# Kernel optimization log

Hardware: AMD Instinct MI355X
Metric: run time of the kernel (lower is better)

The kernel has to match this reference:

```python
import jax, jax.numpy as jnp
import numpy as np

B = 512     # graphs
NPG = 128   # nodes per graph
EPG = 2048  # edges per graph (avg degree 16)
IN = 128
HID = 128
K = 64      # ceil(0.5 * 128), SAGPooling ratio=0.5


def setup_inputs() -> dict:
    key = jax.random.key(0)
    ks = jax.random.split(key, 8)
    n_total = B * NPG
    x = jax.random.normal(ks[0], (n_total, IN), dtype=jnp.float32)
    # intra-graph random edges (PyG batching: edges never cross graphs)
    g = jnp.repeat(jnp.arange(B, dtype=jnp.int32), EPG)
    src = g * NPG + jax.random.randint(ks[1], (B * EPG,), 0, NPG, dtype=jnp.int32)
    dst = g * NPG + jax.random.randint(ks[2], (B * EPG,), 0, NPG, dtype=jnp.int32)
    edge_index = jnp.stack([src, dst], axis=0)
    batch = jnp.repeat(jnp.arange(B, dtype=jnp.int32), NPG)
    # params (glorot-ish scaling)
    W1 = jax.random.normal(ks[3], (IN, HID), dtype=jnp.float32) / np.sqrt(IN)
    b1 = jnp.zeros((HID,), dtype=jnp.float32)
    Ws = jax.random.normal(ks[4], (HID, 1), dtype=jnp.float32) / np.sqrt(HID)
    bs = jnp.zeros((1,), dtype=jnp.float32)
    Wlin = jax.random.normal(ks[5], (HID, HID), dtype=jnp.float32) / np.sqrt(HID)
    blin = jnp.zeros((HID,), dtype=jnp.float32)
    return {"x": x, "edge_index": edge_index, "batch": batch,
            "W1": W1, "b1": b1, "Ws": Ws, "bs": bs, "Wlin": Wlin, "blin": blin}


def _gcn_conv(x, src, dst, W, b, n):
    # PyG GCNConv: add self loops, symmetric deg^-1/2 norm, aggregate src->dst
    h = x @ W  # [n, out]
    loop = jnp.arange(n, dtype=src.dtype)
    s = jnp.concatenate([src, loop])
    d = jnp.concatenate([dst, loop])
    deg = jax.ops.segment_sum(jnp.ones(d.shape[0], dtype=x.dtype), d, num_segments=n)
    norm = jax.lax.rsqrt(deg)[s] * jax.lax.rsqrt(deg)[d]  # deg >= 1 via self loops
    msg = h[s] * norm[:, None]
    return jax.ops.segment_sum(msg, d, num_segments=n) + b


def reference(x, edge_index, batch, W1, b1, Ws, bs, Wlin, blin):
    n = x.shape[0]
    src, dst = edge_index[0], edge_index[1]
    # conv1 + relu
    h = jax.nn.relu(_gcn_conv(x, src, dst, W1, b1, n))  # [n, HID]
    # SAGPooling: score via GCNConv(HID -> 1)
    score = _gcn_conv(h, src, dst, Ws, bs, n)[:, 0]  # [n]
    # per-graph top-k on raw score (graphs are uniform NPG nodes -> dense top_k)
    score2 = score.reshape(B, NPG)
    top_v, top_i = jax.lax.top_k(score2, K)  # [B, K]
    h3 = h.reshape(B, NPG, HID)
    h_kept = jnp.take_along_axis(h3, top_i[:, :, None], axis=1)  # [B, K, HID]
    h_kept = h_kept * jnp.tanh(top_v)[:, :, None]  # x[perm] * tanh(score[perm])
    # global_mean_pool over kept nodes of each graph
    pooled = h_kept.mean(axis=1)  # [B, HID]
    return pooled @ Wlin + blin
```

## Files before the change

kernel.cpp:

```cpp
#include <hip/hip_runtime.h>
#include <math.h>

#define NPG  128
#define HID  128
#define KSEL 64
#define NT   256
#define HS   132
#define AS   17

typedef __attribute__((ext_vector_type(8))) __bf16 bfrag;
typedef __attribute__((ext_vector_type(4))) float f4;

static __device__ __forceinline__ __bf16 us2bf(unsigned short u) {
    union { unsigned short s; __bf16 b; } x; x.s = u; return x.b;
}
static __device__ __forceinline__ unsigned short bf2us(__bf16 b) {
    union { unsigned short s; __bf16 b; } x; x.b = b; return x.s;
}

__global__ __launch_bounds__(64) void wsplit_kernel(const float* __restrict__ W1,
                                                    bfrag* __restrict__ whi,
                                                    bfrag* __restrict__ wlo)
{
    const int b = blockIdx.x;
    const int ks = b >> 3, ct = b & 7;
    const int lane = threadIdx.x;
    const int n = lane & 15, quad = lane >> 4;
    bfrag h, l;
#pragma unroll
    for (int j = 0; j < 8; ++j) {
        const int k = ks * 32 + quad * 8 + j;
        float w = W1[k * HID + ct * 16 + n];
        __bf16 hh = (__bf16)w;
        h[j] = hh;
        l[j] = (__bf16)(w - (float)hh);
    }
    whi[b * 64 + lane] = h;
    wlo[b * 64 + lane] = l;
}

__global__ __launch_bounds__(NT, 2) void sagpool_fused(
    const float* __restrict__ x,
    const int*   __restrict__ esrc,
    const int*   __restrict__ edst,
    const bfrag* __restrict__ whi,
    const bfrag* __restrict__ wlo,
    const float* __restrict__ b1,
    const float* __restrict__ Ws,
    const float* __restrict__ bsp,
    const float* __restrict__ Wlin,
    const float* __restrict__ blin,
    float* __restrict__ out,
    int epg)
{
    __shared__ __align__(16) unsigned HpT[HID * HS];
    __shared__ __align__(16) unsigned AdjN[NPG * AS];
    __shared__ __align__(16) float rsl[NPG];
    __shared__ __align__(16) float spl[NPG];
    __shared__ __align__(16) float scl[NPG];
    __shared__ __align__(16) float wgt[NPG];
    __shared__ __align__(16) float pp[4 * HID];

    const int g = blockIdx.x, t = threadIdx.x;
    const int node0 = g * NPG;
    const long e0 = (long)g * epg;
    const int lane = t & 63, wv = t >> 6;
    const int n16 = lane & 15, quad = lane >> 4;

    int es[8], ed[8];
#pragma unroll
    for (int i = 0; i < 8; ++i) {
        int e = i * NT + t;
        es[i] = esrc[e0 + e] - node0;
        ed[i] = edst[e0 + e] - node0;
    }
    float4 xv[16];
    {
        const float* xw = x + (long)(node0 + wv * 32) * HID;
#pragma unroll
        for (int rt = 0; rt < 2; ++rt)
#pragma unroll
            for (int ks = 0; ks < 4; ++ks) {
                const float* xr = xw + (rt * 16 + n16) * HID + ks * 32 + quad * 8;
                xv[(rt * 4 + ks) * 2]     = *reinterpret_cast<const float4*>(xr);
                xv[(rt * 4 + ks) * 2 + 1] = *reinterpret_cast<const float4*>(xr + 4);
            }
    }
    float b1v[8], wsv[8];
#pragma unroll
    for (int ct = 0; ct < 8; ++ct) {
        b1v[ct] = b1[ct * 16 + n16];
        wsv[ct] = Ws[ct * 16 + n16];
    }
    const float bsv = bsp[0];

    for (int i = t; i < NPG * AS; i += NT) AdjN[i] = 0u;
    __syncthreads();
#pragma unroll
    for (int i = 0; i < 8; ++i)
        atomicAdd(&AdjN[ed[i] * AS + (es[i] >> 3)], 1u << ((es[i] & 7) * 4));
    __syncthreads();

    if (t < NPG) {
        unsigned* row = &AdjN[t * AS];
        row[t >> 3] += 1u << ((t & 7) * 4);
        unsigned sum = 0;
#pragma unroll
        for (int w = 0; w < 16; ++w) {
            unsigned u = row[w];
            unsigned b = (u & 0x0F0F0F0Fu) + ((u >> 4) & 0x0F0F0F0Fu);
            sum += (b * 0x01010101u) >> 24;
        }
        rsl[t] = rsqrtf((float)sum);
    }
    __syncthreads();

    bfrag ah[8], al[8];
#pragma unroll
    for (int r = 0; r < 8; ++r) {
        float4 a = xv[2 * r], b = xv[2 * r + 1];
        float vv[8] = {a.x, a.y, a.z, a.w, b.x, b.y, b.z, b.w};
#pragma unroll
        for (int j = 0; j < 8; ++j) {
            __bf16 hb = (__bf16)vv[j];
            ah[r][j] = hb;
            al[r][j] = (__bf16)(vv[j] - (float)hb);
        }
    }
    f4 acc[2][8];
#pragma unroll
    for (int rt = 0; rt < 2; ++rt)
#pragma unroll
        for (int ct = 0; ct < 8; ++ct) {
            acc[rt][ct].x = 0.f; acc[rt][ct].y = 0.f;
            acc[rt][ct].z = 0.f; acc[rt][ct].w = 0.f;
        }
#pragma unroll
    for (int ks = 0; ks < 4; ++ks)
#pragma unroll
        for (int ct = 0; ct < 8; ++ct) {
            bfrag bh = whi[(ks * 8 + ct) * 64 + lane];
            bfrag bl = wlo[(ks * 8 + ct) * 64 + lane];
#pragma unroll
            for (int rt = 0; rt < 2; ++rt) {
                const int r = rt * 4 + ks;
                acc[rt][ct] = __builtin_amdgcn_mfma_f32_16x16x32_bf16(ah[r], bh, acc[rt][ct], 0, 0, 0);
                acc[rt][ct] = __builtin_amdgcn_mfma_f32_16x16x32_bf16(al[r], bh, acc[rt][ct], 0, 0, 0);
                acc[rt][ct] = __builtin_amdgcn_mfma_f32_16x16x32_bf16(ah[r], bl, acc[rt][ct], 0, 0, 0);
                acc[rt][ct] = __builtin_amdgcn_mfma_f32_16x16x32_bf16(al[r], bl, acc[rt][ct], 0, 0, 0);
            }
        }

#pragma unroll
    for (int rt = 0; rt < 2; ++rt) {
        const int mb = wv * 32 + rt * 16 + quad * 4;
        f4 rs4 = *reinterpret_cast<const f4*>(&rsl[mb]);
#pragma unroll
        for (int ct = 0; ct < 8; ++ct) {
            uint4 st;
            unsigned pw[4];
#pragma unroll
            for (int reg = 0; reg < 4; ++reg) {
                float v = acc[rt][ct][reg] * rs4[reg];
                __bf16 hb = (__bf16)v;
                __bf16 lb = (__bf16)(v - (float)hb);
                pw[reg] = ((unsigned)bf2us(hb) << 16) | (unsigned)bf2us(lb);
            }
            st.x = pw[0]; st.y = pw[1]; st.z = pw[2]; st.w = pw[3];
            *reinterpret_cast<uint4*>(&HpT[(ct * 16 + n16) * HS + mb]) = st;
        }
    }
    __syncthreads();

    f4 hacc[2][8];
#pragma unroll
    for (int mt = 0; mt < 2; ++mt)
#pragma unroll
        for (int ct = 0; ct < 8; ++ct) {
            hacc[mt][ct].x = 0.f; hacc[mt][ct].y = 0.f;
            hacc[mt][ct].z = 0.f; hacc[mt][ct].w = 0.f;
        }
#pragma unroll
    for (int ks = 0; ks < 4; ++ks) {
        bfrag af[2];
#pragma unroll
        for (int mt = 0; mt < 2; ++mt) {
            unsigned w = AdjN[(wv * 32 + mt * 16 + n16) * AS + ks * 4 + quad];
#pragma unroll
            for (int j = 0; j < 8; ++j)
                af[mt][j] = (__bf16)(float)((w >> (4 * j)) & 15u);
        }
#pragma unroll
        for (int ct = 0; ct < 8; ++ct) {
            const unsigned* bp = &HpT[(ct * 16 + n16) * HS + ks * 32 + quad * 8];
            uint4 w0 = *reinterpret_cast<const uint4*>(bp);
            uint4 w1 = *reinterpret_cast<const uint4*>(bp + 4);
            unsigned ww[8] = {w0.x, w0.y, w0.z, w0.w, w1.x, w1.y, w1.z, w1.w};
            bfrag bh, bl;
#pragma unroll
            for (int j = 0; j < 8; ++j) {
                bh[j] = us2bf((unsigned short)(ww[j] >> 16));
                bl[j] = us2bf((unsigned short)(ww[j] & 0xFFFFu));
            }
#pragma unroll
            for (int mt = 0; mt < 2; ++mt) {
                hacc[mt][ct] = __builtin_amdgcn_mfma_f32_16x16x32_bf16(af[mt], bh, hacc[mt][ct], 0, 0, 0);
                hacc[mt][ct] = __builtin_amdgcn_mfma_f32_16x16x32_bf16(af[mt], bl, hacc[mt][ct], 0, 0, 0);
            }
        }
    }

    f4 rsm[2];
#pragma unroll
    for (int mt = 0; mt < 2; ++mt)
        rsm[mt] = *reinterpret_cast<const f4*>(&rsl[wv * 32 + mt * 16 + quad * 4]);
#pragma unroll
    for (int mt = 0; mt < 2; ++mt)
#pragma unroll
        for (int ct = 0; ct < 8; ++ct)
#pragma unroll
            for (int reg = 0; reg < 4; ++reg)
                hacc[mt][ct][reg] = fmaxf(hacc[mt][ct][reg] * rsm[mt][reg] + b1v[ct], 0.f);

    {
        float dot[2][4];
#pragma unroll
        for (int mt = 0; mt < 2; ++mt)
#pragma unroll
            for (int reg = 0; reg < 4; ++reg) dot[mt][reg] = 0.f;
#pragma unroll
        for (int ct = 0; ct < 8; ++ct)
#pragma unroll
            for (int mt = 0; mt < 2; ++mt)
#pragma unroll
                for (int reg = 0; reg < 4; ++reg)
                    dot[mt][reg] += hacc[mt][ct][reg] * wsv[ct];
#pragma unroll
        for (int d = 1; d < 16; d <<= 1)
#pragma unroll
            for (int mt = 0; mt < 2; ++mt)
#pragma unroll
                for (int reg = 0; reg < 4; ++reg)
                    dot[mt][reg] += __shfl_xor(dot[mt][reg], d, 64);
        if (n16 == 0) {
#pragma unroll
            for (int mt = 0; mt < 2; ++mt)
#pragma unroll
                for (int reg = 0; reg < 4; ++reg)
                    spl[wv * 32 + mt * 16 + quad * 4 + reg] = rsm[mt][reg] * dot[mt][reg];
        }
    }
    __syncthreads();

    if (t < NPG) {
        const unsigned* row = &AdjN[t * AS];
        float sc = 0.f;
#pragma unroll
        for (int w = 0; w < 16; ++w) {
            unsigned u = row[w];
            const float* sp = &spl[w * 8];
            sc += (float)(u & 15u)         * sp[0] + (float)((u >> 4)  & 15u) * sp[1]
                + (float)((u >> 8)  & 15u) * sp[2] + (float)((u >> 12) & 15u) * sp[3]
                + (float)((u >> 16) & 15u) * sp[4] + (float)((u >> 20) & 15u) * sp[5]
                + (float)((u >> 24) & 15u) * sp[6] + (float)(u >> 28)         * sp[7];
        }
        scl[t] = rsl[t] * sc + bsv;
    }
    __syncthreads();

    if (t < NPG) {
        float v = scl[t];
        int rank = 0;
        for (int j = 0; j < NPG; ++j) {
            float u = scl[j];
            rank += (u > v || (u == v && j < t)) ? 1 : 0;
        }
        wgt[t] = (rank < KSEL) ? tanhf(v) * (1.0f / KSEL) : 0.f;
    }
    __syncthreads();

    {
        float p[8];
        f4 wm[2];
#pragma unroll
        for (int mt = 0; mt < 2; ++mt)
            wm[mt] = *reinterpret_cast<const f4*>(&wgt[wv * 32 + mt * 16 + quad * 4]);
#pragma unroll
        for (int ct = 0; ct < 8; ++ct) {
            float s = 0.f;
#pragma unroll
            for (int mt = 0; mt < 2; ++mt)
#pragma unroll
                for (int reg = 0; reg < 4; ++reg)
                    s += wm[mt][reg] * hacc[mt][ct][reg];
            p[ct] = s;
        }
#pragma unroll
        for (int d = 16; d < 64; d <<= 1)
#pragma unroll
            for (int ct = 0; ct < 8; ++ct)
                p[ct] += __shfl_xor(p[ct], d, 64);
        if (quad == 0) {
#pragma unroll
            for (int ct = 0; ct < 8; ++ct)
                pp[wv * HID + ct * 16 + n16] = p[ct];
        }
    }
    __syncthreads();
    if (t < NPG)
        scl[t] = pp[t] + pp[HID + t] + pp[2 * HID + t] + pp[3 * HID + t];
    __syncthreads();

    {
        const int c = t & 127, hf = t >> 7;
        float s = 0.f;
        for (int k = hf * 64; k < hf * 64 + 64; ++k)
            s += scl[k] * Wlin[k * HID + c];
        pp[t] = s;
    }
    __syncthreads();
    if (t < NPG)
        out[(long)g * HID + t] = pp[t] + pp[t + 128] + blin[t];
}

extern "C" void kernel_launch(void* const* d_in, const int* in_sizes, int n_in,
                              void* d_out, int out_size, void* d_ws, size_t ws_size,
                              hipStream_t stream) {
    const float* x    = (const float*)d_in[0];
    const int*   ei   = (const int*)  d_in[1];
    const float* W1   = (const float*)d_in[3];
    const float* b1   = (const float*)d_in[4];
    const float* Ws   = (const float*)d_in[5];
    const float* bs   = (const float*)d_in[6];
    const float* Wlin = (const float*)d_in[7];
    const float* blin = (const float*)d_in[8];
    float* out = (float*)d_out;

    const int E = in_sizes[1] / 2;
    const int nnodes = in_sizes[0] / HID;
    const int B = nnodes / NPG;
    const int epg = E / B;

    bfrag* whi = reinterpret_cast<bfrag*>(d_ws);
    bfrag* wlo = whi + 32 * 64;

    wsplit_kernel<<<32, 64, 0, stream>>>(W1, whi, wlo);
    sagpool_fused<<<B, NT, 0, stream>>>(x, ei, ei + E, whi, wlo, b1, Ws, bs,
                                        Wlin, blin, out, epg);
}
```

Baseline: 111.8 us.

## Double block size so each wave processes 16 node rows instead of 32

The fused SAGPool kernel now runs 512 threads per graph instead of 256, and each wave owns one 16-row MFMA tile instead of two. Per-thread register arrays (x fragments, accumulators, edge lists) are halved, and launch bounds ask for 4 blocks per CU. The aim is more active waves to hide latency of the MFMA chains and memory loads. The pooling reduction gains an extra sync so the upper four waves can accumulate into pp, and the final Wlin matvec is split four ways. Shared memory per block is unchanged, so LDS may still cap how many blocks fit on a CU.

```diff
diff --git a/kernel.cpp b/kernel.cpp
--- a/kernel.cpp
+++ b/kernel.cpp
@@ -4,7 +4,7 @@
 #define NPG  128
 #define HID  128
 #define KSEL 64
-#define NT   256
+#define NT   512
 #define HS   132
 #define AS   17
 
@@ -39,7 +39,7 @@
     wlo[b * 64 + lane] = l;
 }
 
-__global__ __launch_bounds__(NT, 2) void sagpool_fused(
+__global__ __launch_bounds__(NT, 4) void sagpool_fused(
     const float* __restrict__ x,
     const int*   __restrict__ esrc,
     const int*   __restrict__ edst,
@@ -66,25 +66,30 @@
     const long e0 = (long)g * epg;
     const int lane = t & 63, wv = t >> 6;
     const int n16 = lane & 15, quad = lane >> 4;
-
-    int es[8], ed[8];
-#pragma unroll
-    for (int i = 0; i < 8; ++i) {
+    const int m0 = wv * 16;
+
+    int es[4], ed[4];
+#pragma unroll
+    for (int i = 0; i < 4; ++i) {
         int e = i * NT + t;
         es[i] = esrc[e0 + e] - node0;
         ed[i] = edst[e0 + e] - node0;
     }
-    float4 xv[16];
-    {
-        const float* xw = x + (long)(node0 + wv * 32) * HID;
-#pragma unroll
-        for (int rt = 0; rt < 2; ++rt)
-#pragma unroll
-            for (int ks = 0; ks < 4; ++ks) {
-                const float* xr = xw + (rt * 16 + n16) * HID + ks * 32 + quad * 8;
-                xv[(rt * 4 + ks) * 2]     = *reinterpret_cast<const float4*>(xr);
-                xv[(rt * 4 + ks) * 2 + 1] = *reinterpret_cast<const float4*>(xr + 4);
+    bfrag ah[4], al[4];
+    {
+        const float* xr0 = x + (long)(node0 + m0 + n16) * HID + quad * 8;
+#pragma unroll
+        for (int ks = 0; ks < 4; ++ks) {
+            float4 a = *reinterpret_cast<const float4*>(xr0 + ks * 32);
+            float4 b = *reinterpret_cast<const float4*>(xr0 + ks * 32 + 4);
+            float vv[8] = {a.x, a.y, a.z, a.w, b.x, b.y, b.z, b.w};
+#pragma unroll
+            for (int j = 0; j < 8; ++j) {
+                __bf16 hb = (__bf16)vv[j];
+                ah[ks][j] = hb;
+                al[ks][j] = (__bf16)(vv[j] - (float)hb);
             }
+        }
     }
     float b1v[8], wsv[8];
 #pragma unroll
@@ -97,7 +102,7 @@
     for (int i = t; i < NPG * AS; i += NT) AdjN[i] = 0u;
     __syncthreads();
 #pragma unroll
-    for (int i = 0; i < 8; ++i)
+    for (int i = 0; i < 4; ++i)
         atomicAdd(&AdjN[ed[i] * AS + (es[i] >> 3)], 1u << ((es[i] & 7) * 4));
     __syncthreads();
 
@@ -115,45 +120,25 @@
     }
     __syncthreads();
 
-    bfrag ah[8], al[8];
-#pragma unroll
-    for (int r = 0; r < 8; ++r) {
-        float4 a = xv[2 * r], b = xv[2 * r + 1];
-        float vv[8] = {a.x, a.y, a.z, a.w, b.x, b.y, b.z, b.w};
-#pragma unroll
-        for (int j = 0; j < 8; ++j) {
-            __bf16 hb = (__bf16)vv[j];
-            ah[r][j] = hb;
-            al[r][j] = (__bf16)(vv[j] - (float)hb);
-        }
-    }
-    f4 acc[2][8];
-#pragma unroll
-    for (int rt = 0; rt < 2; ++rt)
-#pragma unroll
-        for (int ct = 0; ct < 8; ++ct) {
-            acc[rt][ct].x = 0.f; acc[rt][ct].y = 0.f;
-            acc[rt][ct].z = 0.f; acc[rt][ct].w = 0.f;
-        }
+    f4 acc[8];
+#pragma unroll
+    for (int ct = 0; ct < 8; ++ct) {
+        acc[ct].x = 0.f; acc[ct].y = 0.f; acc[ct].z = 0.f; acc[ct].w = 0.f;
+    }
 #pragma unroll
     for (int ks = 0; ks < 4; ++ks)
 #pragma unroll
         for (int ct = 0; ct < 8; ++ct) {
             bfrag bh = whi[(ks * 8 + ct) * 64 + lane];
             bfrag bl = wlo[(ks * 8 + ct) * 64 + lane];
-#pragma unroll
-            for (int rt = 0; rt < 2; ++rt) {
-                const int r = rt * 4 + ks;
-                acc[rt][ct] = __builtin_amdgcn_mfma_f32_16x16x32_bf16(ah[r], bh, acc[rt][ct], 0, 0, 0);
-                acc[rt][ct] = __builtin_amdgcn_mfma_f32_16x16x32_bf16(al[r], bh, acc[rt][ct], 0, 0, 0);
-                acc[rt][ct] = __builtin_amdgcn_mfma_f32_16x16x32_bf16(ah[r], bl, acc[rt][ct], 0, 0, 0);
-                acc[rt][ct] = __builtin_amdgcn_mfma_f32_16x16x32_bf16(al[r], bl, acc[rt][ct], 0, 0, 0);
-            }
-        }
-
-#pragma unroll
-    for (int rt = 0; rt < 2; ++rt) {
-        const int mb = wv * 32 + rt * 16 + quad * 4;
+            acc[ct] = __builtin_amdgcn_mfma_f32_16x16x32_bf16(ah[ks], bh, acc[ct], 0, 0, 0);
+            acc[ct] = __builtin_amdgcn_mfma_f32_16x16x32_bf16(al[ks], bh, acc[ct], 0, 0, 0);
+            acc[ct] = __builtin_amdgcn_mfma_f32_16x16x32_bf16(ah[ks], bl, acc[ct], 0, 0, 0);
+            acc[ct] = __builtin_amdgcn_mfma_f32_16x16x32_bf16(al[ks], bl, acc[ct], 0, 0, 0);
+        }
+
+    {
+        const int mb = m0 + quad * 4;
         f4 rs4 = *reinterpret_cast<const f4*>(&rsl[mb]);
 #pragma unroll
         for (int ct = 0; ct < 8; ++ct) {
@@ -161,7 +146,7 @@
             unsigned pw[4];
 #pragma unroll
             for (int reg = 0; reg < 4; ++reg) {
-                float v = acc[rt][ct][reg] * rs4[reg];
+                float v = acc[ct][reg] * rs4[reg];
                 __bf16 hb = (__bf16)v;
                 __bf16 lb = (__bf16)(v - (float)hb);
                 pw[reg] = ((unsigned)bf2us(hb) << 16) | (unsigned)bf2us(lb);
@@ -172,23 +157,19 @@
     }
     __syncthreads();
 
-    f4 hacc[2][8];
-#pragma unroll
-    for (int mt = 0; mt < 2; ++mt)
-#pragma unroll
-        for (int ct = 0; ct < 8; ++ct) {
-            hacc[mt][ct].x = 0.f; hacc[mt][ct].y = 0.f;
-            hacc[mt][ct].z = 0.f; hacc[mt][ct].w = 0.f;
-        }
+    f4 hacc[8];
+#pragma unroll
+    for (int ct = 0; ct < 8; ++ct) {
+        hacc[ct].x = 0.f; hacc[ct].y = 0.f; hacc[ct].z = 0.f; hacc[ct].w = 0.f;
+    }
 #pragma unroll
     for (int ks = 0; ks < 4; ++ks) {
-        bfrag af[2];
-#pragma unroll
-        for (int mt = 0; mt < 2; ++mt) {
-            unsigned w = AdjN[(wv * 32 + mt * 16 + n16) * AS + ks * 4 + quad];
+        bfrag af;
+        {
+            unsigned w = AdjN[(m0 + n16) * AS + ks * 4 + quad];
 #pragma unroll
             for (int j = 0; j < 8; ++j)
-                af[mt][j] = (__bf16)(float)((w >> (4 * j)) & 15u);
+                af[j] = (__bf16)(float)((w >> (4 * j)) & 15u);
         }
 #pragma unroll
         for (int ct = 0; ct < 8; ++ct) {
@@ -202,52 +183,36 @@
                 bh[j] = us2bf((unsigned short)(ww[j] >> 16));
                 bl[j] = us2bf((unsigned short)(ww[j] & 0xFFFFu));
             }
-#pragma unroll
-            for (int mt = 0; mt < 2; ++mt) {
-                hacc[mt][ct] = __builtin_amdgcn_mfma_f32_16x16x32_bf16(af[mt], bh, hacc[mt][ct], 0, 0, 0);
-                hacc[mt][ct] = __builtin_amdgcn_mfma_f32_16x16x32_bf16(af[mt], bl, hacc[mt][ct], 0, 0, 0);
-            }
-        }
-    }
-
-    f4 rsm[2];
-#pragma unroll
-    for (int mt = 0; mt < 2; ++mt)
-        rsm[mt] = *reinterpret_cast<const f4*>(&rsl[wv * 32 + mt * 16 + quad * 4]);
-#pragma unroll
-    for (int mt = 0; mt < 2; ++mt)
+            hacc[ct] = __builtin_amdgcn_mfma_f32_16x16x32_bf16(af, bh, hacc[ct], 0, 0, 0);
+            hacc[ct] = __builtin_amdgcn_mfma_f32_16x16x32_bf16(af, bl, hacc[ct], 0, 0, 0);
+        }
+    }
+
+    f4 rsm = *reinterpret_cast<const f4*>(&rsl[m0 + quad * 4]);
+#pragma unroll
+    for (int ct = 0; ct < 8; ++ct)
+#pragma unroll
+        for (int reg = 0; reg < 4; ++reg)
+            hacc[ct][reg] = fmaxf(hacc[ct][reg] * rsm[reg] + b1v[ct], 0.f);
+
+    {
+        float dot[4];
+#pragma unroll
+        for (int reg = 0; reg < 4; ++reg) dot[reg] = 0.f;
 #pragma unroll
         for (int ct = 0; ct < 8; ++ct)
 #pragma unroll
             for (int reg = 0; reg < 4; ++reg)
-                hacc[mt][ct][reg] = fmaxf(hacc[mt][ct][reg] * rsm[mt][reg] + b1v[ct], 0.f);
-
-    {
-        float dot[2][4];
-#pragma unroll
-        for (int mt = 0; mt < 2; ++mt)
-#pragma unroll
-            for (int reg = 0; reg < 4; ++reg) dot[mt][reg] = 0.f;
-#pragma unroll
-        for (int ct = 0; ct < 8; ++ct)
-#pragma unroll
-            for (int mt = 0; mt < 2; ++mt)
-#pragma unroll
-                for (int reg = 0; reg < 4; ++reg)
-                    dot[mt][reg] += hacc[mt][ct][reg] * wsv[ct];
+                dot[reg] += hacc[ct][reg] * wsv[ct];
 #pragma unroll
         for (int d = 1; d < 16; d <<= 1)
 #pragma unroll
-            for (int mt = 0; mt < 2; ++mt)
-#pragma unroll
-                for (int reg = 0; reg < 4; ++reg)
-                    dot[mt][reg] += __shfl_xor(dot[mt][reg], d, 64);
+            for (int reg = 0; reg < 4; ++reg)
+                dot[reg] += __shfl_xor(dot[reg], d, 64);
         if (n16 == 0) {
 #pragma unroll
-            for (int mt = 0; mt < 2; ++mt)
-#pragma unroll
-                for (int reg = 0; reg < 4; ++reg)
-                    spl[wv * 32 + mt * 16 + quad * 4 + reg] = rsm[mt][reg] * dot[mt][reg];
+            for (int reg = 0; reg < 4; ++reg)
+                spl[m0 + quad * 4 + reg] = rsm[reg] * dot[reg];
         }
     }
     __syncthreads();
@@ -281,18 +246,13 @@
 
     {
         float p[8];
-        f4 wm[2];
-#pragma unroll
-        for (int mt = 0; mt < 2; ++mt)
-            wm[mt] = *reinterpret_cast<const f4*>(&wgt[wv * 32 + mt * 16 + quad * 4]);
+        f4 wm = *reinterpret_cast<const f4*>(&wgt[m0 + quad * 4]);
 #pragma unroll
         for (int ct = 0; ct < 8; ++ct) {
             float s = 0.f;
 #pragma unroll
-            for (int mt = 0; mt < 2; ++mt)
-#pragma unroll
-                for (int reg = 0; reg < 4; ++reg)
-                    s += wm[mt][reg] * hacc[mt][ct][reg];
+            for (int reg = 0; reg < 4; ++reg)
+                s += wm[reg] * hacc[ct][reg];
             p[ct] = s;
         }
 #pragma unroll
@@ -300,11 +260,17 @@
 #pragma unroll
             for (int ct = 0; ct < 8; ++ct)
                 p[ct] += __shfl_xor(p[ct], d, 64);
-        if (quad == 0) {
+        if (wv < 4 && quad == 0) {
 #pragma unroll
             for (int ct = 0; ct < 8; ++ct)
                 pp[wv * HID + ct * 16 + n16] = p[ct];
         }
+        __syncthreads();
+        if (wv >= 4 && quad == 0) {
+#pragma unroll
+            for (int ct = 0; ct < 8; ++ct)
+                pp[(wv - 4) * HID + ct * 16 + n16] += p[ct];
+        }
     }
     __syncthreads();
     if (t < NPG)
@@ -314,13 +280,13 @@
     {
         const int c = t & 127, hf = t >> 7;
         float s = 0.f;
-        for (int k = hf * 64; k < hf * 64 + 64; ++k)
+        for (int k = hf * 32; k < hf * 32 + 32; ++k)
             s += scl[k] * Wlin[k * HID + c];
         pp[t] = s;
     }
     __syncthreads();
     if (t < NPG)
-        out[(long)g * HID + t] = pp[t] + pp[t + 128] + blin[t];
+        out[(long)g * HID + t] = pp[t] + pp[t + 128] + pp[t + 256] + pp[t + 384] + blin[t];
 }
 
 extern "C" void kernel_launch(void* const* d_in, const int* in_sizes, int n_in,
```

Result: no change. 113.8 us (+1.8%).

## Overlap degree counting with first GEMM, stage Wlin in LDS, vectorize ranking

Applied to the files above, without the earlier changes.

Converts x to split-bf16 fragments right after loading and counts degrees with a separate LDS atomic counter. This lets the first MFMA GEMM start before the adjacency row scan and its barrier, so edge scatter and matrix work overlap. After the HpT buffer is no longer needed, Wlin is copied into it so the final projection reads LDS instead of global memory. The top-k rank loop is unrolled with float4 reads. The cost is extra LDS atomics and a larger staging copy of Wlin per block.

```diff
diff --git a/kernel.cpp b/kernel.cpp
--- a/kernel.cpp
+++ b/kernel.cpp
@@ -55,6 +55,7 @@
 {
     __shared__ __align__(16) unsigned HpT[HID * HS];
     __shared__ __align__(16) unsigned AdjN[NPG * AS];
+    __shared__ __align__(16) int   degl[NPG];
     __shared__ __align__(16) float rsl[NPG];
     __shared__ __align__(16) float spl[NPG];
     __shared__ __align__(16) float scl[NPG];
@@ -66,6 +67,7 @@
     const long e0 = (long)g * epg;
     const int lane = t & 63, wv = t >> 6;
     const int n16 = lane & 15, quad = lane >> 4;
+    const int m0 = wv * 32;
 
     int es[8], ed[8];
 #pragma unroll
@@ -74,16 +76,24 @@
         es[i] = esrc[e0 + e] - node0;
         ed[i] = edst[e0 + e] - node0;
     }
-    float4 xv[16];
-    {
-        const float* xw = x + (long)(node0 + wv * 32) * HID;
+    bfrag ah[8], al[8];
+    {
+        const float* xw = x + (long)(node0 + m0) * HID;
 #pragma unroll
         for (int rt = 0; rt < 2; ++rt)
 #pragma unroll
             for (int ks = 0; ks < 4; ++ks) {
                 const float* xr = xw + (rt * 16 + n16) * HID + ks * 32 + quad * 8;
-                xv[(rt * 4 + ks) * 2]     = *reinterpret_cast<const float4*>(xr);
-                xv[(rt * 4 + ks) * 2 + 1] = *reinterpret_cast<const float4*>(xr + 4);
+                float4 a = *reinterpret_cast<const float4*>(xr);
+                float4 b = *reinterpret_cast<const float4*>(xr + 4);
+                float vv[8] = {a.x, a.y, a.z, a.w, b.x, b.y, b.z, b.w};
+                const int r = rt * 4 + ks;
+#pragma unroll
+                for (int j = 0; j < 8; ++j) {
+                    __bf16 hb = (__bf16)vv[j];
+                    ah[r][j] = hb;
+                    al[r][j] = (__bf16)(vv[j] - (float)hb);
+                }
             }
     }
     float b1v[8], wsv[8];
@@ -95,38 +105,15 @@
     const float bsv = bsp[0];
 
     for (int i = t; i < NPG * AS; i += NT) AdjN[i] = 0u;
-    __syncthreads();
-#pragma unroll
-    for (int i = 0; i < 8; ++i)
+    if (t < NPG) degl[t] = 0;
+    __syncthreads();
+
+#pragma unroll
+    for (int i = 0; i < 8; ++i) {
         atomicAdd(&AdjN[ed[i] * AS + (es[i] >> 3)], 1u << ((es[i] & 7) * 4));
-    __syncthreads();
-
-    if (t < NPG) {
-        unsigned* row = &AdjN[t * AS];
-        row[t >> 3] += 1u << ((t & 7) * 4);
-        unsigned sum = 0;
-#pragma unroll
-        for (int w = 0; w < 16; ++w) {
-            unsigned u = row[w];
-            unsigned b = (u & 0x0F0F0F0Fu) + ((u >> 4) & 0x0F0F0F0Fu);
-            sum += (b * 0x01010101u) >> 24;
-        }
-        rsl[t] = rsqrtf((float)sum);
-    }
-    __syncthreads();
-
-    bfrag ah[8], al[8];
-#pragma unroll
-    for (int r = 0; r < 8; ++r) {
-        float4 a = xv[2 * r], b = xv[2 * r + 1];
-        float vv[8] = {a.x, a.y, a.z, a.w, b.x, b.y, b.z, b.w};
-#pragma unroll
-        for (int j = 0; j < 8; ++j) {
-            __bf16 hb = (__bf16)vv[j];
-            ah[r][j] = hb;
-            al[r][j] = (__bf16)(vv[j] - (float)hb);
-        }
-    }
+        atomicAdd(&degl[ed[i]], 1);
+    }
+
     f4 acc[2][8];
 #pragma unroll
     for (int rt = 0; rt < 2; ++rt)
@@ -150,10 +137,17 @@
                 acc[rt][ct] = __builtin_amdgcn_mfma_f32_16x16x32_bf16(al[r], bl, acc[rt][ct], 0, 0, 0);
             }
         }
+    __syncthreads();
+
+    if (t < NPG) {
+        rsl[t] = rsqrtf((float)(degl[t] + 1));
+        AdjN[t * AS + (t >> 3)] += 1u << ((t & 7) * 4);
+    }
+    __syncthreads();
 
 #pragma unroll
     for (int rt = 0; rt < 2; ++rt) {
-        const int mb = wv * 32 + rt * 16 + quad * 4;
+        const int mb = m0 + rt * 16 + quad * 4;
         f4 rs4 = *reinterpret_cast<const f4*>(&rsl[mb]);
 #pragma unroll
         for (int ct = 0; ct < 8; ++ct) {
@@ -185,7 +179,7 @@
         bfrag af[2];
 #pragma unroll
         for (int mt = 0; mt < 2; ++mt) {
-            unsigned w = AdjN[(wv * 32 + mt * 16 + n16) * AS + ks * 4 + quad];
+            unsigned w = AdjN[(m0 + mt * 16 + n16) * AS + ks * 4 + quad];
 #pragma unroll
             for (int j = 0; j < 8; ++j)
                 af[mt][j] = (__bf16)(float)((w >> (4 * j)) & 15u);
@@ -213,7 +207,7 @@
     f4 rsm[2];
 #pragma unroll
     for (int mt = 0; mt < 2; ++mt)
-        rsm[mt] = *reinterpret_cast<const f4*>(&rsl[wv * 32 + mt * 16 + quad * 4]);
+        rsm[mt] = *reinterpret_cast<const f4*>(&rsl[m0 + mt * 16 + quad * 4]);
 #pragma unroll
     for (int mt = 0; mt < 2; ++mt)
 #pragma unroll
@@ -247,10 +241,18 @@
             for (int mt = 0; mt < 2; ++mt)
 #pragma unroll
                 for (int reg = 0; reg < 4; ++reg)
-                    spl[wv * 32 + mt * 16 + quad * 4 + reg] = rsm[mt][reg] * dot[mt][reg];
-        }
-    }
-    __syncthreads();
+                    spl[m0 + mt * 16 + quad * 4 + reg] = rsm[mt][reg] * dot[mt][reg];
+        }
+    }
+    __syncthreads();
+
+    {
+        float4* WL4 = reinterpret_cast<float4*>(HpT);
+        const float4* Wg4 = reinterpret_cast<const float4*>(Wlin);
+#pragma unroll
+        for (int i = 0; i < 16; ++i)
+            WL4[i * NT + t] = Wg4[i * NT + t];
+    }
 
     if (t < NPG) {
         const unsigned* row = &AdjN[t * AS];
@@ -271,9 +273,14 @@
     if (t < NPG) {
         float v = scl[t];
         int rank = 0;
-        for (int j = 0; j < NPG; ++j) {
-            float u = scl[j];
-            rank += (u > v || (u == v && j < t)) ? 1 : 0;
+#pragma unroll
+        for (int j4 = 0; j4 < 32; ++j4) {
+            float4 u = *reinterpret_cast<const float4*>(&scl[j4 * 4]);
+            const int jb = j4 * 4;
+            rank += (u.x > v || (u.x == v && jb     < t)) ? 1 : 0;
+            rank += (u.y > v || (u.y == v && jb + 1 < t)) ? 1 : 0;
+            rank += (u.z > v || (u.z == v && jb + 2 < t)) ? 1 : 0;
+            rank += (u.w > v || (u.w == v && jb + 3 < t)) ? 1 : 0;
         }
         wgt[t] = (rank < KSEL) ? tanhf(v) * (1.0f / KSEL) : 0.f;
     }
@@ -284,7 +291,7 @@
         f4 wm[2];
 #pragma unroll
         for (int mt = 0; mt < 2; ++mt)
-            wm[mt] = *reinterpret_cast<const f4*>(&wgt[wv * 32 + mt * 16 + quad * 4]);
+            wm[mt] = *reinterpret_cast<const f4*>(&wgt[m0 + mt * 16 + quad * 4]);
 #pragma unroll
         for (int ct = 0; ct < 8; ++ct) {
             float s = 0.f;
@@ -313,9 +320,11 @@
 
     {
         const int c = t & 127, hf = t >> 7;
+        const float* WL = reinterpret_cast<const float*>(HpT);
         float s = 0.f;
+#pragma unroll
         for (int k = hf * 64; k < hf * 64 + 64; ++k)
-            s += scl[k] * Wlin[k * HID + c];
+            s += scl[k] * WL[k * HID + c];
         pp[t] = s;
     }
     __syncthreads();
```

New measurement: 113.1 us. Within noise of the previous version (+1.2%).
